# Optimization experiments

Hardware: AMD Instinct MI355X
Metric: run time of the kernel (lower is better)

Reference implementation:

```python
import jax, jax.numpy as jnp
import numpy as np

N = 50000      # nodes
E = 1600000    # edges (avg degree 32)
F_IN = 256     # input feature dim
H = 128        # hidden == output size of GCN
C = 40         # num_class


def setup_inputs() -> dict:
    key = jax.random.key(0)
    ks = jax.random.split(key, 13)
    inp = {
        "features": jax.random.normal(ks[0], (N, F_IN), dtype=jnp.float32),
        "src": jax.random.randint(ks[1], (E,), 0, N, dtype=jnp.int32),
        "dst": jax.random.randint(ks[2], (E,), 0, N, dtype=jnp.int32),
        "edge_weight": jax.random.uniform(ks[3], (E,), dtype=jnp.float32),
        "y": jax.random.normal(ks[4], (N, C), dtype=jnp.float32),
        # GCN layer 1
        "W1": jax.random.normal(ks[5], (F_IN, H), dtype=jnp.float32) / np.sqrt(F_IN),
        "b1": jnp.zeros((H,), dtype=jnp.float32),
        # GCN layer 2
        "W2": jax.random.normal(ks[6], (H, H), dtype=jnp.float32) / np.sqrt(H),
        "b2": jnp.zeros((H,), dtype=jnp.float32),
        # y_fc_emb: Linear(num_class, output_size)
        "We": jax.random.normal(ks[7], (C, H), dtype=jnp.float32) / np.sqrt(C),
        "be": jnp.zeros((H,), dtype=jnp.float32),
        # y_fc: Linear(hidden*2, num_class)
        "Wf": jax.random.normal(ks[8], (2 * H, C), dtype=jnp.float32) / np.sqrt(2 * H),
        "bf": jnp.zeros((C,), dtype=jnp.float32),
    }
    return inp


def _spmm(edge_weight, src, dst, x, n):
    # (sparse adj) @ x : out[i] = sum_{(j->i)} w_ji * x[j]
    return jax.ops.segment_sum(edge_weight[:, None] * x[src], dst, num_segments=n)


def reference(features, src, dst, edge_weight, y, W1, b1, W2, b2, We, be, Wf, bf):
    n = features.shape[0]
    # F.normalize: L2 row-normalize with eps=1e-12 clamp
    norm = jnp.maximum(jnp.linalg.norm(features, axis=1, keepdims=True), 1e-12)
    x = features / norm
    # GCN layer 1: relu(adj @ (x @ W1) + b1)   (dropout = 0)
    h = jax.nn.relu(_spmm(edge_weight, src, dst, x @ W1, n) + b1)
    # GCN layer 2: adj @ (h @ W2) + b2
    h = _spmm(edge_weight, src, dst, h @ W2, n) + b2
    # label embedding + head
    y_emb = y @ We + be
    logits = jnp.concatenate([y_emb, h], axis=1) @ Wf + bf
    return jax.nn.softmax(logits, axis=-1)
```

## Files before the change

kernel.cpp:

```cpp
#include <hip/hip_runtime.h>
#include <hip/hip_bf16.h>
#include <hip/hip_fp16.h>
#include <cstdint>
#include <cstddef>
#include <cmath>

#define F_IN 256
#define HDIM 128
#define CCLS 40
#define NBMAX 1024
#define EPB_H 16384
#define EPB 8192

typedef short bf16x8 __attribute__((ext_vector_type(8)));
typedef float f32x4 __attribute__((ext_vector_type(4)));

__device__ inline unsigned pkbf(float a, float b) {
  __hip_bfloat162 h = __float22bfloat162_rn(make_float2(a, b));
  unsigned u;
  __builtin_memcpy(&u, &h, 4);
  return u;
}
__device__ inline unsigned short bfr(float f) {
  __hip_bfloat16 h = __float2bfloat16(f);
  unsigned short u;
  __builtin_memcpy(&u, &h, 2);
  return u;
}
__device__ inline float f16tof(unsigned short hb) {
  __half hv;
  __builtin_memcpy(&hv, &hb, 2);
  return __half2float(hv);
}
__device__ inline unsigned short ftof16(float f) {
  __half hv = __float2half(f);
  unsigned short u;
  __builtin_memcpy(&u, &hv, 2);
  return u;
}

__global__ __launch_bounds__(256) void prep_kernel(const float* __restrict__ W1,
                                                   unsigned short* __restrict__ W1T,
                                                   const int* __restrict__ dst,
                                                   int* __restrict__ gcount,
                                                   int e, int nb) {
  const int b = blockIdx.x;
  const int t = threadIdx.x;
  if (b < 128) {
    int idx = b * 256 + t;
    int nr = idx >> 8, k = idx & 255;
    W1T[idx] = bfr(W1[k * 128 + nr]);
  } else {
    __shared__ int h[NBMAX];
    for (int i = t; i < nb; i += 256) h[i] = 0;
    __syncthreads();
    int b4 = (b - 128) * (EPB_H / 4);
#pragma unroll
    for (int k = 0; k < EPB_H / 1024; ++k) {
      int gi = b4 + k * 256 + t;
      int e0 = gi * 4;
      int4 d = make_int4(-1, -1, -1, -1);
      if (e0 + 3 < e) d = ((const int4*)dst)[gi];
      else if (e0 < e) {
        d.x = dst[e0];
        if (e0 + 1 < e) d.y = dst[e0 + 1];
        if (e0 + 2 < e) d.z = dst[e0 + 2];
      }
      if (d.x >= 0) atomicAdd(&h[d.x >> 6], 1);
      if (d.y >= 0) atomicAdd(&h[d.y >> 6], 1);
      if (d.z >= 0) atomicAdd(&h[d.z >> 6], 1);
      if (d.w >= 0) atomicAdd(&h[d.w >> 6], 1);
    }
    __syncthreads();
    for (int i = t; i < nb; i += 256)
      if (h[i]) atomicAdd(&gcount[i], h[i]);
  }
}

__global__ __launch_bounds__(256) void scatter_gemm1(const int* __restrict__ src,
                                                     const int* __restrict__ dst,
                                                     const float* __restrict__ w,
                                                     const int* __restrict__ gcount,
                                                     int* __restrict__ gcursor,
                                                     uint2* __restrict__ ews,
                                                     const float* __restrict__ X,
                                                     const unsigned short* __restrict__ W1T,
                                                     unsigned short* __restrict__ C,
                                                     const float* __restrict__ W2,
                                                     unsigned short* __restrict__ W2T,
                                                     const float* __restrict__ We,
                                                     const float* __restrict__ be,
                                                     const float* __restrict__ Wf,
                                                     const float* __restrict__ bf,
                                                     float* __restrict__ Wc,
                                                     float* __restrict__ bc,
                                                     int e, int nb, int nsb, int ngb,
                                                     int M) {
  __shared__ char smem[3 * NBMAX * 4 + 256 * 4];
  const int t = threadIdx.x;
  const int b = blockIdx.x;
  if (b < nsb) {
    int* hist = (int*)smem;
    int* sb   = hist + NBMAX;
    int* lcur = sb + NBMAX;
    int* part = lcur + NBMAX;
    for (int i = t; i < nb; i += 256) { hist[i] = 0; lcur[i] = 0; }
    __syncthreads();
    const int b4 = b * (EPB / 4);
#pragma unroll
    for (int k = 0; k < 8; ++k) {
      int gi = b4 + k * 256 + t;
      int e0 = gi * 4;
      if (e0 >= e) continue;
      int4 d = make_int4(-1, -1, -1, -1);
      if (e0 + 3 < e) d = ((const int4*)dst)[gi];
      else {
        d.x = dst[e0];
        if (e0 + 1 < e) d.y = dst[e0 + 1];
        if (e0 + 2 < e) d.z = dst[e0 + 2];
      }
      if (d.x >= 0) atomicAdd(&hist[d.x >> 6], 1);
      if (d.y >= 0) atomicAdd(&hist[d.y >> 6], 1);
      if (d.z >= 0) atomicAdd(&hist[d.z >> 6], 1);
      if (d.w >= 0) atomicAdd(&hist[d.w >> 6], 1);
    }
    __syncthreads();
    int v[4];
    int s = 0;
#pragma unroll
    for (int k = 0; k < 4; ++k) {
      int i = t * 4 + k;
      v[k] = (i < nb) ? gcount[i] : 0;
      s += v[k];
    }
    part[t] = s;
    __syncthreads();
    for (int off = 1; off < 256; off <<= 1) {
      int x = part[t];
      if (t >= off) x += part[t - off];
      __syncthreads();
      part[t] = x;
      __syncthreads();
    }
    int run = (t == 0) ? 0 : part[t - 1];
#pragma unroll
    for (int k = 0; k < 4; ++k) {
      int i = t * 4 + k;
      if (i < nb) sb[i] = run;
      run += v[k];
    }
    __syncthreads();
    for (int i = t; i < nb; i += 256) {
      int c = hist[i];
      sb[i] = sb[i] + (c ? atomicAdd(&gcursor[i], c) : 0);
    }
    __syncthreads();
#pragma unroll
    for (int k = 0; k < 8; ++k) {
      int gi = b4 + k * 256 + t;
      int e0 = gi * 4;
      if (e0 >= e) continue;
      int4 d = make_int4(-1, -1, -1, -1);
      int4 s4 = make_int4(0, 0, 0, 0);
      float4 w4 = make_float4(0.f, 0.f, 0.f, 0.f);
      if (e0 + 3 < e) {
        d = ((const int4*)dst)[gi];
        s4 = ((const int4*)src)[gi];
        w4 = ((const float4*)w)[gi];
      } else {
        d.x = dst[e0]; s4.x = src[e0]; w4.x = w[e0];
        if (e0 + 1 < e) { d.y = dst[e0 + 1]; s4.y = src[e0 + 1]; w4.y = w[e0 + 1]; }
        if (e0 + 2 < e) { d.z = dst[e0 + 2]; s4.z = src[e0 + 2]; w4.z = w[e0 + 2]; }
      }
      if (d.x >= 0) { int bb = d.x >> 6; int r = atomicAdd(&lcur[bb], 1);
        ews[sb[bb] + r] = make_uint2(((unsigned)(d.x & 63) << 26) | (unsigned)s4.x, __float_as_uint(w4.x)); }
      if (d.y >= 0) { int bb = d.y >> 6; int r = atomicAdd(&lcur[bb], 1);
        ews[sb[bb] + r] = make_uint2(((unsigned)(d.y & 63) << 26) | (unsigned)s4.y, __float_as_uint(w4.y)); }
      if (d.z >= 0) { int bb = d.z >> 6; int r = atomicAdd(&lcur[bb], 1);
        ews[sb[bb] + r] = make_uint2(((unsigned)(d.z & 63) << 26) | (unsigned)s4.z, __float_as_uint(w4.z)); }
      if (d.w >= 0) { int bb = d.w >> 6; int r = atomicAdd(&lcur[bb], 1);
        ews[sb[bb] + r] = make_uint2(((unsigned)(d.w & 63) << 26) | (unsigned)s4.w, __float_as_uint(w4.w)); }
    }
  } else if (b < nsb + ngb) {
    unsigned short (*As)[264] = (unsigned short(*)[264])smem;
    const int w8 = t >> 6, l = t & 63;
    const int bm0 = (b - nsb) * 16;
    for (int rr = 0; rr < 4; ++rr) {
      int row = w8 * 4 + rr;
      int grow = bm0 + row;
      const float* p = X + (size_t)(grow < M ? grow : (M - 1)) * F_IN + l * 4;
      float4 v = *(const float4*)p;
      float s = v.x * v.x + v.y * v.y + v.z * v.z + v.w * v.w;
#pragma unroll
      for (int off = 32; off; off >>= 1) s += __shfl_xor(s, off, 64);
      float inv = 1.0f / fmaxf(sqrtf(s), 1e-12f);
      *(uint2*)&As[row][l * 4] =
          make_uint2(pkbf(v.x * inv, v.y * inv), pkbf(v.z * inv, v.w * inv));
    }
    __syncthreads();
    const int ln = l & 15, quad = l >> 4;
    f32x4 acc[2];
    acc[0] = (f32x4){0.f, 0.f, 0.f, 0.f};
    acc[1] = (f32x4){0.f, 0.f, 0.f, 0.f};
#pragma unroll
    for (int k0 = 0; k0 < F_IN; k0 += 32) {
      bf16x8 af = *(const bf16x8*)&As[ln][k0 + quad * 8];
#pragma unroll
      for (int ti = 0; ti < 2; ++ti) {
        bf16x8 bfv = *(const bf16x8*)(W1T + (size_t)(w8 * 32 + ti * 16 + ln) * F_IN +
                                      k0 + quad * 8);
        acc[ti] = __builtin_amdgcn_mfma_f32_16x16x32_bf16(af, bfv, acc[ti], 0, 0, 0);
      }
    }
#pragma unroll
    for (int r = 0; r < 4; ++r) {
      int grow = bm0 + quad * 4 + r;
      if (grow < M) {
#pragma unroll
        for (int ti = 0; ti < 2; ++ti)
          C[(size_t)grow * HDIM + w8 * 32 + ti * 16 + ln] = bfr(acc[ti][r]);
      }
    }
  } else if (b < nsb + ngb + 64) {
    int idx = (b - nsb - ngb) * 256 + t;
    int nr = idx >> 7, k = idx & 127;
    W2T[idx] = bfr(W2[k * 128 + nr]);
  } else {
    int part = b - (nsb + ngb + 64);
    int lo = part * 800, hi = lo + 800;
    for (int i = lo + t; i < hi; i += 256) {
      int c = i / CCLS, j = i % CCLS;
      float s = 0.f;
      for (int f = 0; f < HDIM; ++f) s += We[c * HDIM + f] * Wf[f * CCLS + j];
      Wc[i] = s;
    }
    if (part == 0 && t < CCLS) {
      float s = bf[t];
      for (int f = 0; f < HDIM; ++f) s += be[f] * Wf[f * CCLS + t];
      bc[t] = s;
    }
  }
}

__global__ __launch_bounds__(256) void bucket_sort(const uint2* __restrict__ ews,
                                                   const int* __restrict__ gcount,
                                                   unsigned* __restrict__ ews2,
                                                   int* __restrict__ row_off,
                                                   int* __restrict__ row_end,
                                                   int n, int nb) {
  __shared__ int cnt[256];
  __shared__ int cur[64];
  __shared__ int sred[4];
  const int t = threadIdx.x;
  const int b = blockIdx.x;
  int partial = 0;
  for (int i = t; i < b; i += 256) partial += gcount[i];
#pragma unroll
  for (int off = 32; off; off >>= 1) partial += __shfl_xor(partial, off, 64);
  if ((t & 63) == 0) sred[t >> 6] = partial;
  cnt[t] = 0;
  __syncthreads();
  const int e0 = sred[0] + sred[1] + sred[2] + sred[3];
  const int e1 = e0 + gcount[b];
  const int wv = t >> 6;
  for (int i = e0 + t; i < e1; i += 256)
    atomicAdd(&cnt[wv * 64 + ((unsigned)ews[i].x >> 26)], 1);
  __syncthreads();
  if (t < 64) {
    int tot = cnt[t] + cnt[64 + t] + cnt[128 + t] + cnt[192 + t];
    int x = tot;
#pragma unroll
    for (int off = 1; off < 64; off <<= 1) {
      int y = __shfl_up(x, off, 64);
      if (t >= off) x += y;
    }
    int excl = x - tot;
    cur[t] = excl;
    int node = b * 64 + t;
    if (node < n) { row_off[node] = e0 + excl; row_end[node] = e0 + excl + tot; }
  }
  __syncthreads();
  for (int i = e0 + t; i < e1; i += 256) {
    uint2 p = ews[i];
    int d = (unsigned)p.x >> 26;
    int pos = e0 + atomicAdd(&cur[d], 1);
    ews2[pos] = (p.x & 0xFFFFu) | ((unsigned)ftof16(__uint_as_float(p.y)) << 16);
  }
}

#define SPMM_PAIR(ua, ub)                                                      \
  {                                                                            \
    unsigned u = half ? (ub) : (ua);                                           \
    float wt = f16tof((unsigned short)(u >> 16));                              \
    const uint2 xv = *(const uint2*)(xin + (size_t)(u & 0xFFFFu) * HDIM + fo); \
    acc.x = fmaf(wt, __uint_as_float(xv.x << 16), acc.x);                      \
    acc.y = fmaf(wt, __uint_as_float(xv.x & 0xFFFF0000u), acc.y);              \
    acc.z = fmaf(wt, __uint_as_float(xv.y << 16), acc.z);                      \
    acc.w = fmaf(wt, __uint_as_float(xv.y & 0xFFFF0000u), acc.w);              \
  }

#define SPMM_NODE_LOOP(ep, cnt)                                                 \
  int k = 0;                                                                    \
  for (; k + 16 <= cnt; k += 16) {                                              \
    unsigned a0 = ep[k + 0], a1 = ep[k + 1], a2 = ep[k + 2], a3 = ep[k + 3];    \
    unsigned a4 = ep[k + 4], a5 = ep[k + 5], a6 = ep[k + 6], a7 = ep[k + 7];    \
    unsigned a8 = ep[k + 8], a9 = ep[k + 9], a10 = ep[k + 10], a11 = ep[k + 11];\
    unsigned a12 = ep[k + 12], a13 = ep[k + 13], a14 = ep[k + 14],              \
             a15 = ep[k + 15];                                                  \
    SPMM_PAIR(a0, a1); SPMM_PAIR(a2, a3); SPMM_PAIR(a4, a5); SPMM_PAIR(a6, a7); \
    SPMM_PAIR(a8, a9); SPMM_PAIR(a10, a11); SPMM_PAIR(a12, a13);                \
    SPMM_PAIR(a14, a15);                                                        \
  }                                                                             \
  for (; k + 8 <= cnt; k += 8) {                                                \
    unsigned a0 = ep[k + 0], a1 = ep[k + 1], a2 = ep[k + 2], a3 = ep[k + 3];    \
    unsigned a4 = ep[k + 4], a5 = ep[k + 5], a6 = ep[k + 6], a7 = ep[k + 7];    \
    SPMM_PAIR(a0, a1); SPMM_PAIR(a2, a3); SPMM_PAIR(a4, a5); SPMM_PAIR(a6, a7); \
  }                                                                             \
  for (; k < cnt; k += 2) {                                                     \
    unsigned a0 = ep[k];                                                        \
    unsigned a1 = (k + 1 < cnt) ? ep[k + 1] : 0u;                               \
    SPMM_PAIR(a0, a1);                                                          \
  }

__global__ __launch_bounds__(256) void spmm1_gemm2(const unsigned short* __restrict__ xin,
                                                   const unsigned* __restrict__ ews,
                                                   const int* __restrict__ row_off,
                                                   const int* __restrict__ row_end,
                                                   const float* __restrict__ bias,
                                                   const unsigned short* __restrict__ W2T,
                                                   unsigned short* __restrict__ C,
                                                   int n) {
  __shared__ unsigned short As[16][136];
  const int t = threadIdx.x;
  const int l = t & 63;
  const int w = t >> 6;
  const int fo = (l & 31) * 4;
  const int half = l >> 5;
  const int nb0 = blockIdx.x * 16;
#pragma unroll
  for (int j = 0; j < 4; ++j) {
    const int node = nb0 + w * 4 + j;
    if (node < n) {
      const int ue0 = __builtin_amdgcn_readfirstlane(row_off[node]);
      const int ue1 = __builtin_amdgcn_readfirstlane(row_end[node]);
      const int cnt = ue1 - ue0;
      const unsigned* ep = ews + ue0;
      float4 acc = make_float4(0.f, 0.f, 0.f, 0.f);
      SPMM_NODE_LOOP(ep, cnt)
      acc.x += __shfl_xor(acc.x, 32, 64);
      acc.y += __shfl_xor(acc.y, 32, 64);
      acc.z += __shfl_xor(acc.z, 32, 64);
      acc.w += __shfl_xor(acc.w, 32, 64);
      if (l < 32) {
        float4 bv = *(const float4*)(bias + fo);
        float r0 = fmaxf(acc.x + bv.x, 0.f), r1 = fmaxf(acc.y + bv.y, 0.f);
        float r2 = fmaxf(acc.z + bv.z, 0.f), r3 = fmaxf(acc.w + bv.w, 0.f);
        *(uint2*)&As[w * 4 + j][fo] = make_uint2(pkbf(r0, r1), pkbf(r2, r3));
      }
    }
  }
  __syncthreads();
  const int ln = l & 15, quad = l >> 4;
  f32x4 acc2[2];
  acc2[0] = (f32x4){0.f, 0.f, 0.f, 0.f};
  acc2[1] = (f32x4){0.f, 0.f, 0.f, 0.f};
#pragma unroll
  for (int k0 = 0; k0 < HDIM; k0 += 32) {
    bf16x8 af = *(const bf16x8*)&As[ln][k0 + quad * 8];
#pragma unroll
    for (int ti = 0; ti < 2; ++ti) {
      bf16x8 bfv = *(const bf16x8*)(W2T + (size_t)(w * 32 + ti * 16 + ln) * HDIM +
                                    k0 + quad * 8);
      acc2[ti] = __builtin_amdgcn_mfma_f32_16x16x32_bf16(af, bfv, acc2[ti], 0, 0, 0);
    }
  }
#pragma unroll
  for (int r = 0; r < 4; ++r) {
    int grow = nb0 + quad * 4 + r;
    if (grow < n) {
#pragma unroll
      for (int ti = 0; ti < 2; ++ti)
        C[(size_t)grow * HDIM + w * 32 + ti * 16 + ln] = bfr(acc2[ti][r]);
    }
  }
}

__global__ __launch_bounds__(256) void spmm_f32(const unsigned short* __restrict__ xin,
                                                const unsigned* __restrict__ ews,
                                                const int* __restrict__ row_off,
                                                const int* __restrict__ row_end,
                                                const float* __restrict__ bias,
                                                float* __restrict__ outp, int n) {
  const int t = threadIdx.x;
  const int l = t & 63;
  const int node = blockIdx.x * 4 + (t >> 6);
  if (node >= n) return;
  const int ue0 = __builtin_amdgcn_readfirstlane(row_off[node]);
  const int ue1 = __builtin_amdgcn_readfirstlane(row_end[node]);
  const int cnt = ue1 - ue0;
  const unsigned* ep = ews + ue0;
  const int fo = (l & 31) * 4;
  const int half = l >> 5;
  float4 acc = make_float4(0.f, 0.f, 0.f, 0.f);
  SPMM_NODE_LOOP(ep, cnt)
  acc.x += __shfl_xor(acc.x, 32, 64);
  acc.y += __shfl_xor(acc.y, 32, 64);
  acc.z += __shfl_xor(acc.z, 32, 64);
  acc.w += __shfl_xor(acc.w, 32, 64);
  if (l < 32) {
    float4 bv = *(const float4*)(bias + fo);
    *(float4*)(outp + (size_t)node * HDIM + fo) =
        make_float4(acc.x + bv.x, acc.y + bv.y, acc.z + bv.z, acc.w + bv.w);
  }
}

__global__ __launch_bounds__(256) void head_kernel(const float* __restrict__ y,
                                                   const float* __restrict__ h2,
                                                   const float* __restrict__ Wc,
                                                   const float* __restrict__ bc,
                                                   const float* __restrict__ Wf,
                                                   float* __restrict__ out, int n) {
  __shared__ float sW[169 * CCLS];
  const int t = threadIdx.x;
  for (int i = t; i < 400; i += 256) ((float4*)sW)[i] = ((const float4*)Wc)[i];
  for (int i = t; i < 1280; i += 256)
    ((float4*)(sW + CCLS * CCLS))[i] = ((const float4*)(Wf + HDIM * CCLS))[i];
  if (t < 10) ((float4*)(sW + 168 * CCLS))[t] = ((const float4*)bc)[t];
  __syncthreads();

  const int node = blockIdx.x * 256 + t;
  const int nc = node < n ? node : n - 1;
  const float* zy = y + (size_t)nc * CCLS;
  const float* zh = h2 + (size_t)nc * HDIM;

  float acc[40];
#pragma unroll
  for (int cq = 0; cq < 10; ++cq) {
    float4 b4 = *(const float4*)&sW[168 * CCLS + cq * 4];
    acc[cq * 4 + 0] = b4.x; acc[cq * 4 + 1] = b4.y;
    acc[cq * 4 + 2] = b4.z; acc[cq * 4 + 3] = b4.w;
  }

#pragma unroll 2
  for (int kc = 0; kc < 10; ++kc) {
    float4 zv = *(const float4*)(zy + kc * 4);
    float zj[4] = {zv.x, zv.y, zv.z, zv.w};
#pragma unroll
    for (int j = 0; j < 4; ++j) {
      const float* wr = sW + (kc * 4 + j) * CCLS;
#pragma unroll
      for (int cq = 0; cq < 10; ++cq) {
        float4 w4 = *(const float4*)(wr + cq * 4);
        acc[cq * 4 + 0] = fmaf(zj[j], w4.x, acc[cq * 4 + 0]);
        acc[cq * 4 + 1] = fmaf(zj[j], w4.y, acc[cq * 4 + 1]);
        acc[cq * 4 + 2] = fmaf(zj[j], w4.z, acc[cq * 4 + 2]);
        acc[cq * 4 + 3] = fmaf(zj[j], w4.w, acc[cq * 4 + 3]);
      }
    }
  }
#pragma unroll 2
  for (int kc = 0; kc < 32; ++kc) {
    float4 zv = *(const float4*)(zh + kc * 4);
    float zj[4] = {zv.x, zv.y, zv.z, zv.w};
#pragma unroll
    for (int j = 0; j < 4; ++j) {
      const float* wr = sW + (40 + kc * 4 + j) * CCLS;
#pragma unroll
      for (int cq = 0; cq < 10; ++cq) {
        float4 w4 = *(const float4*)(wr + cq * 4);
        acc[cq * 4 + 0] = fmaf(zj[j], w4.x, acc[cq * 4 + 0]);
        acc[cq * 4 + 1] = fmaf(zj[j], w4.y, acc[cq * 4 + 1]);
        acc[cq * 4 + 2] = fmaf(zj[j], w4.z, acc[cq * 4 + 2]);
        acc[cq * 4 + 3] = fmaf(zj[j], w4.w, acc[cq * 4 + 3]);
      }
    }
  }

  float m = acc[0];
#pragma unroll
  for (int c = 1; c < 40; ++c) m = fmaxf(m, acc[c]);
  float sum = 0.f;
#pragma unroll
  for (int c = 0; c < 40; ++c) { acc[c] = __expf(acc[c] - m); sum += acc[c]; }
  float inv = 1.0f / sum;
  if (node < n) {
    float* op = out + (size_t)node * CCLS;
#pragma unroll
    for (int cq = 0; cq < 10; ++cq) {
      float4 o = make_float4(acc[cq * 4 + 0] * inv, acc[cq * 4 + 1] * inv,
                             acc[cq * 4 + 2] * inv, acc[cq * 4 + 3] * inv);
      *(float4*)(op + cq * 4) = o;
    }
  }
}

extern "C" void kernel_launch(void* const* d_in, const int* in_sizes, int n_in,
                              void* d_out, int out_size, void* d_ws, size_t ws_size,
                              hipStream_t stream) {
  (void)n_in; (void)out_size; (void)ws_size;
  const float* features = (const float*)d_in[0];
  const int*   src      = (const int*)d_in[1];
  const int*   dst      = (const int*)d_in[2];
  const float* ew       = (const float*)d_in[3];
  const float* y        = (const float*)d_in[4];
  const float* W1       = (const float*)d_in[5];
  const float* b1       = (const float*)d_in[6];
  const float* W2       = (const float*)d_in[7];
  const float* b2       = (const float*)d_in[8];
  const float* We       = (const float*)d_in[9];
  const float* be       = (const float*)d_in[10];
  const float* Wf       = (const float*)d_in[11];
  const float* bf       = (const float*)d_in[12];
  float* out = (float*)d_out;

  const int n = in_sizes[0] / F_IN;
  const int e = in_sizes[1];
  const int nb = (n + 63) >> 6;
  const int hb  = (e + EPB_H - 1) / EPB_H;
  const int nsb = (e + EPB - 1) / EPB;
  const int ngb = (n + 15) / 16;

  char* w = (char*)d_ws;
  auto take = [&](size_t bytes) {
    char* p = w;
    w += (bytes + 255) & ~(size_t)255;
    return p;
  };
  int*   gz       = (int*)take((size_t)2 * nb * 4);
  int*   gcount   = gz;
  int*   gcursor  = gz + nb;
  int*   row_off  = (int*)take((size_t)n * 4);
  int*   row_end  = (int*)take((size_t)n * 4);
  uint2* ews      = (uint2*)take((size_t)e * 8);
  unsigned* ews2  = (unsigned*)take((size_t)(e + 16) * 4);
  unsigned short* bufH1  = (unsigned short*)take((size_t)n * HDIM * 2);
  unsigned short* bufH2  = (unsigned short*)take((size_t)n * HDIM * 2);
  float* bufS     = (float*)take((size_t)n * HDIM * 4);
  unsigned short* W1T = (unsigned short*)take((size_t)HDIM * F_IN * 2);
  unsigned short* W2T = (unsigned short*)take((size_t)HDIM * HDIM * 2);
  float* Wc       = (float*)take(CCLS * CCLS * 4);
  float* bc       = (float*)take(CCLS * 4);

  hipMemsetAsync(gz, 0, (size_t)2 * nb * 4, stream);
  prep_kernel<<<128 + hb, 256, 0, stream>>>(W1, W1T, dst, gcount, e, nb);
  scatter_gemm1<<<nsb + ngb + 64 + 2, 256, 0, stream>>>(
      src, dst, ew, gcount, gcursor, ews, features, W1T, bufH1,
      W2, W2T, We, be, Wf, bf, Wc, bc, e, nb, nsb, ngb, n);
  bucket_sort<<<nb, 256, 0, stream>>>(ews, gcount, ews2, row_off, row_end, n, nb);

  spmm1_gemm2<<<(n + 15) / 16, 256, 0, stream>>>(bufH1, ews2, row_off, row_end, b1,
                                                 W2T, bufH2, n);
  spmm_f32<<<(n + 3) / 4, 256, 0, stream>>>(bufH2, ews2, row_off, row_end, b2, bufS, n);
  head_kernel<<<(n + 255) / 256, 256, 0, stream>>>(y, bufS, Wc, bc, Wf, out, n);
}
```

Before: 332.4 us.

## Fuse second SpMM with softmax head and reuse dst loads in scatter

Merges the layer-2 SpMM and the classification head into one kernel. Each wave aggregates a node's 128-wide row into shared memory, then computes 40 logits (y@Wc + h2@Wf + bc) with one lane per class and does a wave-level softmax. This removes the fp32 intermediate buffer round trip and one launch, but each block now loads about 27KB of weights into LDS for only 16 nodes, and the per-lane head loops are serial. Separately, the scatter kernel keeps the dst values from the histogram pass in registers instead of reloading them.

New measurement: 359.4 us. 1.08x slower.

```diff
diff --git a/kernel.cpp b/kernel.cpp
--- a/kernel.cpp
+++ b/kernel.cpp
@@ -107,18 +107,19 @@
     for (int i = t; i < nb; i += 256) { hist[i] = 0; lcur[i] = 0; }
     __syncthreads();
     const int b4 = b * (EPB / 4);
+    int4 dv[8];
 #pragma unroll
     for (int k = 0; k < 8; ++k) {
       int gi = b4 + k * 256 + t;
       int e0 = gi * 4;
-      if (e0 >= e) continue;
       int4 d = make_int4(-1, -1, -1, -1);
       if (e0 + 3 < e) d = ((const int4*)dst)[gi];
-      else {
+      else if (e0 < e) {
         d.x = dst[e0];
         if (e0 + 1 < e) d.y = dst[e0 + 1];
         if (e0 + 2 < e) d.z = dst[e0 + 2];
       }
+      dv[k] = d;
       if (d.x >= 0) atomicAdd(&hist[d.x >> 6], 1);
       if (d.y >= 0) atomicAdd(&hist[d.y >> 6], 1);
       if (d.z >= 0) atomicAdd(&hist[d.z >> 6], 1);
@@ -160,18 +161,15 @@
       int gi = b4 + k * 256 + t;
       int e0 = gi * 4;
       if (e0 >= e) continue;
-      int4 d = make_int4(-1, -1, -1, -1);
       int4 s4 = make_int4(0, 0, 0, 0);
       float4 w4 = make_float4(0.f, 0.f, 0.f, 0.f);
-      if (e0 + 3 < e) {
-        d = ((const int4*)dst)[gi];
-        s4 = ((const int4*)src)[gi];
-        w4 = ((const float4*)w)[gi];
-      } else {
-        d.x = dst[e0]; s4.x = src[e0]; w4.x = w[e0];
-        if (e0 + 1 < e) { d.y = dst[e0 + 1]; s4.y = src[e0 + 1]; w4.y = w[e0 + 1]; }
-        if (e0 + 2 < e) { d.z = dst[e0 + 2]; s4.z = src[e0 + 2]; w4.z = w[e0 + 2]; }
+      if (e0 + 3 < e) { s4 = ((const int4*)src)[gi]; w4 = ((const float4*)w)[gi]; }
+      else {
+        s4.x = src[e0]; w4.x = w[e0];
+        if (e0 + 1 < e) { s4.y = src[e0 + 1]; w4.y = w[e0 + 1]; }
+        if (e0 + 2 < e) { s4.z = src[e0 + 2]; w4.z = w[e0 + 2]; }
       }
+      int4 d = dv[k];
       if (d.x >= 0) { int bb = d.x >> 6; int r = atomicAdd(&lcur[bb], 1);
         ews[sb[bb] + r] = make_uint2(((unsigned)(d.x & 63) << 26) | (unsigned)s4.x, __float_as_uint(w4.x)); }
       if (d.y >= 0) { int bb = d.y >> 6; int r = atomicAdd(&lcur[bb], 1);
@@ -385,112 +383,71 @@
   }
 }
 
-__global__ __launch_bounds__(256) void spmm_f32(const unsigned short* __restrict__ xin,
-                                                const unsigned* __restrict__ ews,
-                                                const int* __restrict__ row_off,
-                                                const int* __restrict__ row_end,
-                                                const float* __restrict__ bias,
-                                                float* __restrict__ outp, int n) {
+__global__ __launch_bounds__(256) void spmm2_head(const unsigned short* __restrict__ xin,
+                                                  const unsigned* __restrict__ ews,
+                                                  const int* __restrict__ row_off,
+                                                  const int* __restrict__ row_end,
+                                                  const float* __restrict__ b2,
+                                                  const float* __restrict__ y,
+                                                  const float* __restrict__ Wc,
+                                                  const float* __restrict__ bc,
+                                                  const float* __restrict__ Wf,
+                                                  float* __restrict__ out, int n) {
+  __shared__ float sWc[CCLS * CCLS];
+  __shared__ float sWfb[HDIM * CCLS];
+  __shared__ float sbc[CCLS];
+  __shared__ float h2s[4][HDIM];
   const int t = threadIdx.x;
   const int l = t & 63;
-  const int node = blockIdx.x * 4 + (t >> 6);
-  if (node >= n) return;
-  const int ue0 = __builtin_amdgcn_readfirstlane(row_off[node]);
-  const int ue1 = __builtin_amdgcn_readfirstlane(row_end[node]);
-  const int cnt = ue1 - ue0;
-  const unsigned* ep = ews + ue0;
+  const int w = t >> 6;
   const int fo = (l & 31) * 4;
   const int half = l >> 5;
-  float4 acc = make_float4(0.f, 0.f, 0.f, 0.f);
-  SPMM_NODE_LOOP(ep, cnt)
-  acc.x += __shfl_xor(acc.x, 32, 64);
-  acc.y += __shfl_xor(acc.y, 32, 64);
-  acc.z += __shfl_xor(acc.z, 32, 64);
-  acc.w += __shfl_xor(acc.w, 32, 64);
-  if (l < 32) {
-    float4 bv = *(const float4*)(bias + fo);
-    *(float4*)(outp + (size_t)node * HDIM + fo) =
-        make_float4(acc.x + bv.x, acc.y + bv.y, acc.z + bv.z, acc.w + bv.w);
-  }
-}
-
-__global__ __launch_bounds__(256) void head_kernel(const float* __restrict__ y,
-                                                   const float* __restrict__ h2,
-                                                   const float* __restrict__ Wc,
-                                                   const float* __restrict__ bc,
-                                                   const float* __restrict__ Wf,
-                                                   float* __restrict__ out, int n) {
-  __shared__ float sW[169 * CCLS];
-  const int t = threadIdx.x;
-  for (int i = t; i < 400; i += 256) ((float4*)sW)[i] = ((const float4*)Wc)[i];
+  const int nb0 = blockIdx.x * 16;
+  for (int i = t; i < 400; i += 256) ((float4*)sWc)[i] = ((const float4*)Wc)[i];
   for (int i = t; i < 1280; i += 256)
-    ((float4*)(sW + CCLS * CCLS))[i] = ((const float4*)(Wf + HDIM * CCLS))[i];
-  if (t < 10) ((float4*)(sW + 168 * CCLS))[t] = ((const float4*)bc)[t];
+    ((float4*)sWfb)[i] = ((const float4*)(Wf + HDIM * CCLS))[i];
+  if (t < 10) ((float4*)sbc)[t] = ((const float4*)bc)[t];
   __syncthreads();
 
-  const int node = blockIdx.x * 256 + t;
-  const int nc = node < n ? node : n - 1;
-  const float* zy = y + (size_t)nc * CCLS;
-  const float* zh = h2 + (size_t)nc * HDIM;
-
-  float acc[40];
-#pragma unroll
-  for (int cq = 0; cq < 10; ++cq) {
-    float4 b4 = *(const float4*)&sW[168 * CCLS + cq * 4];
-    acc[cq * 4 + 0] = b4.x; acc[cq * 4 + 1] = b4.y;
-    acc[cq * 4 + 2] = b4.z; acc[cq * 4 + 3] = b4.w;
-  }
-
-#pragma unroll 2
-  for (int kc = 0; kc < 10; ++kc) {
-    float4 zv = *(const float4*)(zy + kc * 4);
-    float zj[4] = {zv.x, zv.y, zv.z, zv.w};
-#pragma unroll
-    for (int j = 0; j < 4; ++j) {
-      const float* wr = sW + (kc * 4 + j) * CCLS;
-#pragma unroll
-      for (int cq = 0; cq < 10; ++cq) {
-        float4 w4 = *(const float4*)(wr + cq * 4);
-        acc[cq * 4 + 0] = fmaf(zj[j], w4.x, acc[cq * 4 + 0]);
-        acc[cq * 4 + 1] = fmaf(zj[j], w4.y, acc[cq * 4 + 1]);
-        acc[cq * 4 + 2] = fmaf(zj[j], w4.z, acc[cq * 4 + 2]);
-        acc[cq * 4 + 3] = fmaf(zj[j], w4.w, acc[cq * 4 + 3]);
-      }
-    }
-  }
-#pragma unroll 2
-  for (int kc = 0; kc < 32; ++kc) {
-    float4 zv = *(const float4*)(zh + kc * 4);
-    float zj[4] = {zv.x, zv.y, zv.z, zv.w};
-#pragma unroll
-    for (int j = 0; j < 4; ++j) {
-      const float* wr = sW + (40 + kc * 4 + j) * CCLS;
-#pragma unroll
-      for (int cq = 0; cq < 10; ++cq) {
-        float4 w4 = *(const float4*)(wr + cq * 4);
-        acc[cq * 4 + 0] = fmaf(zj[j], w4.x, acc[cq * 4 + 0]);
-        acc[cq * 4 + 1] = fmaf(zj[j], w4.y, acc[cq * 4 + 1]);
-        acc[cq * 4 + 2] = fmaf(zj[j], w4.z, acc[cq * 4 + 2]);
-        acc[cq * 4 + 3] = fmaf(zj[j], w4.w, acc[cq * 4 + 3]);
-      }
-    }
-  }
-
-  float m = acc[0];
-#pragma unroll
-  for (int c = 1; c < 40; ++c) m = fmaxf(m, acc[c]);
-  float sum = 0.f;
-#pragma unroll
-  for (int c = 0; c < 40; ++c) { acc[c] = __expf(acc[c] - m); sum += acc[c]; }
-  float inv = 1.0f / sum;
-  if (node < n) {
-    float* op = out + (size_t)node * CCLS;
-#pragma unroll
-    for (int cq = 0; cq < 10; ++cq) {
-      float4 o = make_float4(acc[cq * 4 + 0] * inv, acc[cq * 4 + 1] * inv,
-                             acc[cq * 4 + 2] * inv, acc[cq * 4 + 3] * inv);
-      *(float4*)(op + cq * 4) = o;
-    }
+#pragma unroll
+  for (int j = 0; j < 4; ++j) {
+    const int node = nb0 + w * 4 + j;
+    if (node >= n) continue;
+    const int ue0 = __builtin_amdgcn_readfirstlane(row_off[node]);
+    const int ue1 = __builtin_amdgcn_readfirstlane(row_end[node]);
+    const int cnt = ue1 - ue0;
+    const unsigned* ep = ews + ue0;
+    float4 acc = make_float4(0.f, 0.f, 0.f, 0.f);
+    SPMM_NODE_LOOP(ep, cnt)
+    acc.x += __shfl_xor(acc.x, 32, 64);
+    acc.y += __shfl_xor(acc.y, 32, 64);
+    acc.z += __shfl_xor(acc.z, 32, 64);
+    acc.w += __shfl_xor(acc.w, 32, 64);
+    if (l < 32) {
+      float4 bv = *(const float4*)(b2 + fo);
+      h2s[w][fo + 0] = acc.x + bv.x;
+      h2s[w][fo + 1] = acc.y + bv.y;
+      h2s[w][fo + 2] = acc.z + bv.z;
+      h2s[w][fo + 3] = acc.w + bv.w;
+    }
+    float yv = (l < CCLS) ? y[(size_t)node * CCLS + l] : 0.f;
+    float lg = (l < CCLS) ? sbc[l] : -1e30f;
+    if (l < CCLS) {
+#pragma unroll 8
+      for (int ky = 0; ky < CCLS; ++ky)
+        lg = fmaf(__shfl(yv, ky, 64), sWc[ky * CCLS + l], lg);
+#pragma unroll 8
+      for (int k2 = 0; k2 < HDIM; ++k2)
+        lg = fmaf(h2s[w][k2], sWfb[k2 * CCLS + l], lg);
+    }
+    float m = lg;
+#pragma unroll
+    for (int off = 32; off; off >>= 1) m = fmaxf(m, __shfl_xor(m, off, 64));
+    float p = (l < CCLS) ? __expf(lg - m) : 0.f;
+    float sum = p;
+#pragma unroll
+    for (int off = 32; off; off >>= 1) sum += __shfl_xor(sum, off, 64);
+    if (l < CCLS) out[(size_t)node * CCLS + l] = p / sum;
   }
 }
 
@@ -535,7 +492,6 @@
   unsigned* ews2  = (unsigned*)take((size_t)(e + 16) * 4);
   unsigned short* bufH1  = (unsigned short*)take((size_t)n * HDIM * 2);
   unsigned short* bufH2  = (unsigned short*)take((size_t)n * HDIM * 2);
-  float* bufS     = (float*)take((size_t)n * HDIM * 4);
   unsigned short* W1T = (unsigned short*)take((size_t)HDIM * F_IN * 2);
   unsigned short* W2T = (unsigned short*)take((size_t)HDIM * HDIM * 2);
   float* Wc       = (float*)take(CCLS * CCLS * 4);
@@ -550,6 +506,6 @@
 
   spmm1_gemm2<<<(n + 15) / 16, 256, 0, stream>>>(bufH1, ews2, row_off, row_end, b1,
                                                  W2T, bufH2, n);
-  spmm_f32<<<(n + 3) / 4, 256, 0, stream>>>(bufH2, ews2, row_off, row_end, b2, bufS, n);
-  head_kernel<<<(n + 255) / 256, 256, 0, stream>>>(y, bufS, Wc, bc, Wf, out, n);
-}
+  spmm2_head<<<(n + 15) / 16, 256, 0, stream>>>(bufH2, ews2, row_off, row_end, b2,
+                                                y, Wc, bc, Wf, out, n);
+}
```
